# Kernel tuning notes

Hardware: AMD Instinct MI355X
Metric: run time of the kernel (lower is better)

Reference implementation:

```python
import jax, jax.numpy as jnp
import numpy as np

NUM_HEADS = 16
HEAD_DIM = 64
SCALE = HEAD_DIM ** -0.5


def setup_inputs() -> dict:
    key = jax.random.key(0)
    ks = jax.random.split(key, 5)
    B, N, C = 2, 2048, 1024
    x = jax.random.normal(ks[0], (B, N, C), dtype=jnp.float32)
    rel_pos_bias = jax.random.normal(ks[1], (NUM_HEADS, N, N), dtype=jnp.float32) * 0.02
    qkv_w = jax.random.normal(ks[2], (3 * C, C), dtype=jnp.float32) * (C ** -0.5)
    q_bias = jnp.zeros((C,), dtype=jnp.float32)
    v_bias = jnp.zeros((C,), dtype=jnp.float32)
    proj_w = jax.random.normal(ks[3], (C, C), dtype=jnp.float32) * (C ** -0.5)
    proj_b = jnp.zeros((C,), dtype=jnp.float32)
    return {"x": x, "rel_pos_bias": rel_pos_bias, "qkv_w": qkv_w,
            "q_bias": q_bias, "v_bias": v_bias, "proj_w": proj_w, "proj_b": proj_b}


def reference(x, rel_pos_bias, qkv_w, q_bias, v_bias, proj_w, proj_b):
    B, N, C = x.shape
    H, D = NUM_HEADS, HEAD_DIM
    # qkv bias = concat(q_bias, zeros, v_bias)
    qkv_b = jnp.concatenate([q_bias, jnp.zeros_like(v_bias), v_bias])
    qkv = x @ qkv_w.T + qkv_b                       # [B, N, 3C]
    qkv = qkv.reshape(B, N, 3, H, D).transpose(2, 0, 3, 1, 4)  # [3, B, H, N, D]
    q, k, v = qkv[0], qkv[1], qkv[2]
    q = q * SCALE
    attn = jnp.einsum('bhnd,bhmd->bhnm', q, k)      # [B, H, N, N]
    attn = attn + rel_pos_bias[None]                # bias broadcast over batch
    attn = jax.nn.softmax(attn, axis=-1)
    out = jnp.einsum('bhnm,bhmd->bhnd', attn, v)    # [B, H, N, D]
    out = out.transpose(0, 2, 1, 3).reshape(B, N, H * D)
    out = out @ proj_w.T + proj_b
    return out
```

## Files before the change

### kernel.cpp

```cpp
#include <hip/hip_runtime.h>

typedef unsigned short u16;
typedef short bfrag __attribute__((ext_vector_type(8)));
typedef float facc  __attribute__((ext_vector_type(4)));

#define LOG2E 1.44269504088896340736f

static __device__ __forceinline__ float bf2f(u16 b) {
  union { unsigned u; float f; } v; v.u = ((unsigned)b) << 16; return v.f;
}
static __device__ __forceinline__ u16 f2bf(float x) {
  union { float f; unsigned u; } v; v.f = x;
  return (u16)((v.u + 0x7FFFu + ((v.u >> 16) & 1u)) >> 16);
}
static __device__ __forceinline__ void gload_lds16(const u16* g, u16* l) {
  __builtin_amdgcn_global_load_lds((const __attribute__((address_space(1))) void*)g,
                                   (__attribute__((address_space(3))) void*)l,
                                   16, 0, 0);
}
static __device__ __forceinline__ void gload_lds16f(const float* g, float* l) {
  __builtin_amdgcn_global_load_lds((const __attribute__((address_space(1))) void*)g,
                                   (__attribute__((address_space(3))) void*)l,
                                   16, 0, 0);
}

__global__ __launch_bounds__(256) void convert_kernel(
    const float* __restrict__ x, const float* __restrict__ qw, const float* __restrict__ pw,
    u16* __restrict__ xb, u16* __restrict__ qwb, u16* __restrict__ pwb)
{
  const int NX = 4 * 1024 * 1024, NQ = 3 * 1024 * 1024, NP = 1024 * 1024;
  const int total4 = (NX + NQ + NP) >> 2;
  for (int i = blockIdx.x * blockDim.x + threadIdx.x; i < total4;
       i += gridDim.x * blockDim.x) {
    const int e = i << 2;
    const float* s; u16* d; int off;
    if (e < NX)            { s = x;  d = xb;  off = e; }
    else if (e < NX + NQ)  { s = qw; d = qwb; off = e - NX; }
    else                   { s = pw; d = pwb; off = e - NX - NQ; }
    float4 v = *(const float4*)(s + off);
    ushort4 o;
    o.x = f2bf(v.x); o.y = f2bf(v.y); o.z = f2bf(v.z); o.w = f2bf(v.w);
    *(ushort4*)(d + off) = o;
  }
}

static __device__ __forceinline__ void gemm128_bt(
    const u16* __restrict__ A, const u16* __restrict__ B, int K,
    int m0, int n0, u16* As, u16* Bs, facc acc[4][4])
{
  const int lane = threadIdx.x & 63;
  const int wv   = threadIdx.x >> 6;
  const int quad = lane >> 4;
  const int l15  = lane & 15;
  const int wm = wv >> 1, wn = wv & 1;
  const int srow = lane >> 2;
  const int skb  = (lane & 3) * 8;

  facc zero = {0.f, 0.f, 0.f, 0.f};
#pragma unroll
  for (int i = 0; i < 4; ++i)
#pragma unroll
    for (int j = 0; j < 4; ++j) acc[i][j] = zero;

  const int nIter = K >> 5;
  for (int kk = 0; kk < nIter; ++kk) {
    const int k0 = kk << 5;
    __syncthreads();
#pragma unroll
    for (int c = 0; c < 2; ++c) {
      const int seg = wv * 2 + c;
      gload_lds16(A + (long)(m0 + seg * 16 + srow) * K + k0 + skb, As + seg * 512);
      gload_lds16(B + (long)(n0 + seg * 16 + srow) * K + k0 + skb, Bs + seg * 512);
    }
    __syncthreads();
    bfrag af[4], bf[4];
#pragma unroll
    for (int i = 0; i < 4; ++i)
      af[i] = *(const bfrag*)(As + (wm * 64 + i * 16 + l15) * 32 + quad * 8);
#pragma unroll
    for (int j = 0; j < 4; ++j)
      bf[j] = *(const bfrag*)(Bs + (wn * 64 + j * 16 + l15) * 32 + quad * 8);
#pragma unroll
    for (int i = 0; i < 4; ++i)
#pragma unroll
      for (int j = 0; j < 4; ++j)
        acc[i][j] = __builtin_amdgcn_mfma_f32_16x16x32_bf16(af[i], bf[j], acc[i][j], 0, 0, 0);
  }
}

__global__ __launch_bounds__(256) void qkv_gemm_kernel(
    const u16* __restrict__ x, const u16* __restrict__ w,
    const float* __restrict__ qb, const float* __restrict__ vb,
    u16* __restrict__ Q, u16* __restrict__ Kd, u16* __restrict__ Vt)
{
  __shared__ u16 As[128 * 32];
  __shared__ u16 Bs[128 * 32];
  facc acc[4][4];
  const int m0 = blockIdx.y * 128;
  const int n0 = blockIdx.x * 128;
  gemm128_bt(x, w, 1024, m0, n0, As, Bs, acc);

  const int lane = threadIdx.x & 63;
  const int wv = threadIdx.x >> 6;
  const int quad = lane >> 4, l15 = lane & 15;
  const int wm = wv >> 1, wn = wv & 1;
  const int ncb = n0 + wn * 64;
  const int which = ncb >> 10;
  const int h = (ncb >> 6) & 15;

#pragma unroll
  for (int j = 0; j < 4; ++j) {
    const int d = j * 16 + l15;
    const int n_g = ncb + d;
#pragma unroll
    for (int i = 0; i < 4; ++i) {
      const int mg0 = m0 + wm * 64 + i * 16 + quad * 4;
      const int b  = mg0 >> 11;
      const int ns = mg0 & 2047;
      if (which == 0) {
        const float qbv = qb[n_g];
#pragma unroll
        for (int r = 0; r < 4; ++r)
          Q[(((long)(b * 16 + h) * 2048 + ns + r) << 6) + d] =
              f2bf((acc[i][j][r] + qbv) * 0.125f);
      } else if (which == 1) {
#pragma unroll
        for (int r = 0; r < 4; ++r)
          Kd[(((long)(b * 16 + h) * 2048 + ns + r) << 6) + d] = f2bf(acc[i][j][r]);
      } else {
        const float vbv = vb[n_g - 2048];
        ushort4 pk;
        pk.x = f2bf(acc[i][j][0] + vbv);
        pk.y = f2bf(acc[i][j][1] + vbv);
        pk.z = f2bf(acc[i][j][2] + vbv);
        pk.w = f2bf(acc[i][j][3] + vbv);
        *(ushort4*)(Vt + (((long)((b * 16 + h) * 64 + d)) << 11) + ns) = pk;
      }
    }
  }
}

__global__ __launch_bounds__(256, 4) void attn_kernel(
    const u16* __restrict__ Q, const u16* __restrict__ Kd, const u16* __restrict__ Vt,
    const float* __restrict__ bias, u16* __restrict__ AO)
{
  __shared__ u16 P[4][16 * 64];
  __shared__ float BiasS[4][2][16 * 64];
  const int lane = threadIdx.x & 63;
  const int wv = threadIdx.x >> 6;
  const int quad = lane >> 4, l15 = lane & 15;
  int bid = blockIdx.x;
  bid = (bid & 7) * 128 + (bid >> 3);
  const int bh = bid >> 5;
  const int qt = bid & 31;
  const int h = bh & 15;
  const int b = bh >> 4;
  const int q0 = qt * 64 + wv * 16;
  const long baseN = (long)bh << 17;

  bfrag qf0 = *(const bfrag*)(Q + baseN + (long)(q0 + l15) * 64 + quad * 8);
  bfrag qf1 = *(const bfrag*)(Q + baseN + (long)(q0 + l15) * 64 + 32 + quad * 8);

  facc o[4];
  float m_i[4], l_i[4];
  facc zero = {0.f, 0.f, 0.f, 0.f};
#pragma unroll
  for (int t = 0; t < 4; ++t) o[t] = zero;
#pragma unroll
  for (int r = 0; r < 4; ++r) { m_i[r] = -1e30f; l_i[r] = 0.f; }

  const float* brow = bias + ((long)h << 22) + ((long)q0 << 11);
  char* PwB = (char*)&P[wv][0];
  float* bS[2] = { &BiasS[wv][0][0], &BiasS[wv][1][0] };

#pragma unroll
  for (int c = 0; c < 4; ++c)
    gload_lds16f(brow + (long)(c * 4 + quad) * 2048 + l15 * 4, bS[0] + c * 256);

  for (int k0 = 0; k0 < 2048; k0 += 64) {
    const float* bsCur = bS[(k0 >> 6) & 1];
    facc s[4];
#pragma unroll
    for (int kt = 0; kt < 4; ++kt) {
      const u16* kb = Kd + baseN + (long)(k0 + kt * 16 + l15) * 64;
      bfrag kf0 = *(const bfrag*)(kb + quad * 8);
      bfrag kf1 = *(const bfrag*)(kb + 32 + quad * 8);
      facc z = zero;
      z = __builtin_amdgcn_mfma_f32_16x16x32_bf16(qf0, kf0, z, 0, 0, 0);
      z = __builtin_amdgcn_mfma_f32_16x16x32_bf16(qf1, kf1, z, 0, 0, 0);
      s[kt] = z;
    }
    asm volatile("s_waitcnt vmcnt(0)" ::: "memory");
#pragma unroll
    for (int kt = 0; kt < 4; ++kt)
#pragma unroll
      for (int r = 0; r < 4; ++r)
        s[kt][r] += bsCur[(quad * 4 + r) * 64 + kt * 16 + l15];

    if (k0 + 64 < 2048) {
      float* bsNxt = bS[((k0 >> 6) + 1) & 1];
      const float* src = brow + k0 + 64;
#pragma unroll
      for (int c = 0; c < 4; ++c)
        gload_lds16f(src + (long)(c * 4 + quad) * 2048 + l15 * 4, bsNxt + c * 256);
    }

    float alpha[4];
#pragma unroll
    for (int r = 0; r < 4; ++r) {
      float v = fmaxf(fmaxf(s[0][r], s[1][r]), fmaxf(s[2][r], s[3][r]));
      v = fmaxf(v, __shfl_xor(v, 1, 16));
      v = fmaxf(v, __shfl_xor(v, 2, 16));
      v = fmaxf(v, __shfl_xor(v, 4, 16));
      v = fmaxf(v, __shfl_xor(v, 8, 16));
      const float mn = fmaxf(m_i[r], v);
      alpha[r] = exp2f((m_i[r] - mn) * LOG2E);
      m_i[r] = mn;
    }
#pragma unroll
    for (int r = 0; r < 4; ++r) {
      const float p0 = exp2f((s[0][r] - m_i[r]) * LOG2E);
      const float p1 = exp2f((s[1][r] - m_i[r]) * LOG2E);
      const float p2 = exp2f((s[2][r] - m_i[r]) * LOG2E);
      const float p3 = exp2f((s[3][r] - m_i[r]) * LOG2E);
      s[0][r] = p0; s[1][r] = p1; s[2][r] = p2; s[3][r] = p3;
      float v = (p0 + p1) + (p2 + p3);
      v += __shfl_xor(v, 1, 16);
      v += __shfl_xor(v, 2, 16);
      v += __shfl_xor(v, 4, 16);
      v += __shfl_xor(v, 8, 16);
      l_i[r] = l_i[r] * alpha[r] + v;
    }
#pragma unroll
    for (int t = 0; t < 4; ++t)
#pragma unroll
      for (int r = 0; r < 4; ++r) o[t][r] *= alpha[r];

#pragma unroll
    for (int kt = 0; kt < 4; ++kt)
#pragma unroll
      for (int r = 0; r < 4; ++r) {
        const int bo = (kt * 2 + (l15 >> 3)) * 256 + (quad * 4 + r) * 16 + (l15 & 7) * 2;
        *(u16*)(PwB + bo) = f2bf(s[kt][r]);
      }

#pragma unroll
    for (int p = 0; p < 2; ++p) {
      bfrag pfp = *(const bfrag*)(PwB + p * 1024 + lane * 16);
#pragma unroll
      for (int t = 0; t < 4; ++t) {
        bfrag vf = *(const bfrag*)(Vt + baseN + (((long)(t * 16 + l15)) << 11)
                                   + k0 + p * 32 + quad * 8);
        o[t] = __builtin_amdgcn_mfma_f32_16x16x32_bf16(pfp, vf, o[t], 0, 0, 0);
      }
    }
  }

#pragma unroll
  for (int r = 0; r < 4; ++r) l_i[r] = 1.0f / l_i[r];
#pragma unroll
  for (int t = 0; t < 4; ++t)
#pragma unroll
    for (int r = 0; r < 4; ++r) {
      const int row = q0 + quad * 4 + r;
      AO[(((long)(b * 2048 + row)) << 10) + h * 64 + t * 16 + l15] = f2bf(o[t][r] * l_i[r]);
    }
}

__global__ __launch_bounds__(256) void proj_kernel(
    const u16* __restrict__ Ain, const u16* __restrict__ w,
    const float* __restrict__ pb, float* __restrict__ out)
{
  __shared__ u16 As[128 * 32];
  __shared__ u16 Bs[128 * 32];
  facc acc[4][4];
  const int m0 = blockIdx.y * 128;
  const int n0 = blockIdx.x * 128;
  gemm128_bt(Ain, w, 1024, m0, n0, As, Bs, acc);

  const int lane = threadIdx.x & 63;
  const int wv = threadIdx.x >> 6;
  const int quad = lane >> 4, l15 = lane & 15;
  const int wm = wv >> 1, wn = wv & 1;
#pragma unroll
  for (int j = 0; j < 4; ++j) {
    const int n_g = n0 + wn * 64 + j * 16 + l15;
    const float pbv = pb[n_g];
#pragma unroll
    for (int i = 0; i < 4; ++i) {
      const int mg0 = m0 + wm * 64 + i * 16 + quad * 4;
#pragma unroll
      for (int r = 0; r < 4; ++r)
        out[(((long)(mg0 + r)) << 10) + n_g] = acc[i][j][r] + pbv;
    }
  }
}

extern "C" void kernel_launch(void* const* d_in, const int* in_sizes, int n_in,
                              void* d_out, int out_size, void* d_ws, size_t ws_size,
                              hipStream_t stream)
{
  const float* x    = (const float*)d_in[0];
  const float* bias = (const float*)d_in[1];
  const float* qkvw = (const float*)d_in[2];
  const float* qb   = (const float*)d_in[3];
  const float* vb   = (const float*)d_in[4];
  const float* pw   = (const float*)d_in[5];
  const float* pb   = (const float*)d_in[6];
  float* out = (float*)d_out;

  char* ws = (char*)d_ws;
  u16* Q    = (u16*)(ws);
  u16* Kd   = (u16*)(ws + (size_t)8  * 1024 * 1024);
  u16* Vt   = (u16*)(ws + (size_t)16 * 1024 * 1024);
  u16* AO   = (u16*)(ws + (size_t)24 * 1024 * 1024);
  u16* xb   = (u16*)(ws + (size_t)32 * 1024 * 1024);
  u16* qwb  = (u16*)(ws + (size_t)40 * 1024 * 1024);
  u16* pwb  = (u16*)(ws + (size_t)46 * 1024 * 1024);

  hipLaunchKernelGGL(convert_kernel, dim3(1024), dim3(256), 0, stream,
                     x, qkvw, pw, xb, qwb, pwb);
  hipLaunchKernelGGL(qkv_gemm_kernel, dim3(24, 32), dim3(256), 0, stream,
                     xb, qwb, qb, vb, Q, Kd, Vt);
  hipLaunchKernelGGL(attn_kernel, dim3(1024), dim3(256), 0, stream,
                     Q, Kd, Vt, bias, AO);
  hipLaunchKernelGGL(proj_kernel, dim3(8, 32), dim3(256), 0, stream,
                     AO, pwb, pb, out);
}
```

Measured before the change: 671.8 us.

## Split attention over key halves, share bias across batch, add combine kernel

The attention kernel now splits the key dimension in two (split-K) and writes unnormalized partial outputs plus max and sum to a workspace. A new combine kernel merges them into the bf16 attention output. Each block pairs the two batch elements for the same head and query rows so the rel_pos_bias tile is loaded once and shared, using a swizzled LDS layout, non-temporal loads and a block-wide barrier. Occupancy is raised to 8 waves per SIMD. This trades an extra kernel launch and a partial-output round trip for more parallelism and half the bias traffic.

```diff
diff --git a/kernel.cpp b/kernel.cpp
--- a/kernel.cpp
+++ b/kernel.cpp
@@ -6,9 +6,6 @@
 
 #define LOG2E 1.44269504088896340736f
 
-static __device__ __forceinline__ float bf2f(u16 b) {
-  union { unsigned u; float f; } v; v.u = ((unsigned)b) << 16; return v.f;
-}
 static __device__ __forceinline__ u16 f2bf(float x) {
   union { float f; unsigned u; } v; v.f = x;
   return (u16)((v.u + 0x7FFFu + ((v.u >> 16) & 1u)) >> 16);
@@ -18,10 +15,10 @@
                                    (__attribute__((address_space(3))) void*)l,
                                    16, 0, 0);
 }
-static __device__ __forceinline__ void gload_lds16f(const float* g, float* l) {
+static __device__ __forceinline__ void gload_lds16f_nt(const float* g, float* l) {
   __builtin_amdgcn_global_load_lds((const __attribute__((address_space(1))) void*)g,
                                    (__attribute__((address_space(3))) void*)l,
-                                   16, 0, 0);
+                                   16, 0, 2);
 }
 
 __global__ __launch_bounds__(256) void convert_kernel(
@@ -140,26 +137,29 @@
   }
 }
 
-__global__ __launch_bounds__(256, 4) void attn_kernel(
+__global__ __launch_bounds__(256, 8) void attn_kernel(
     const u16* __restrict__ Q, const u16* __restrict__ Kd, const u16* __restrict__ Vt,
-    const float* __restrict__ bias, u16* __restrict__ AO)
+    const float* __restrict__ bias, float* __restrict__ Part)
 {
   __shared__ u16 P[4][16 * 64];
-  __shared__ float BiasS[4][2][16 * 64];
+  __shared__ float BiasS[2][2][16 * 64];
   const int lane = threadIdx.x & 63;
   const int wv = threadIdx.x >> 6;
   const int quad = lane >> 4, l15 = lane & 15;
-  int bid = blockIdx.x;
-  bid = (bid & 7) * 128 + (bid >> 3);
-  const int bh = bid >> 5;
-  const int qt = bid & 31;
-  const int h = bh & 15;
-  const int b = bh >> 4;
-  const int q0 = qt * 64 + wv * 16;
+  const int L  = (blockIdx.x & 7) * 256 + (blockIdx.x >> 3);
+  const int h  = L >> 7;
+  const int ks = (L >> 6) & 1;
+  const int qg = L & 63;
+  const int q0 = qg * 32;
+  const int b  = wv & 1;
+  const int qh = wv >> 1;
+  const int bh = b * 16 + h;
+  const int qw = q0 + qh * 16;
+  const int ksBase = ks << 10;
   const long baseN = (long)bh << 17;
 
-  bfrag qf0 = *(const bfrag*)(Q + baseN + (long)(q0 + l15) * 64 + quad * 8);
-  bfrag qf1 = *(const bfrag*)(Q + baseN + (long)(q0 + l15) * 64 + 32 + quad * 8);
+  bfrag qf0 = *(const bfrag*)(Q + baseN + (long)(qw + l15) * 64 + quad * 8);
+  bfrag qf1 = *(const bfrag*)(Q + baseN + (long)(qw + l15) * 64 + 32 + quad * 8);
 
   facc o[4];
   float m_i[4], l_i[4];
@@ -169,16 +169,26 @@
 #pragma unroll
   for (int r = 0; r < 4; ++r) { m_i[r] = -1e30f; l_i[r] = 0.f; }
 
-  const float* brow = bias + ((long)h << 22) + ((long)q0 << 11);
+  const float* bh_bias = bias + ((long)h << 22) + ((long)q0 << 11);
   char* PwB = (char*)&P[wv][0];
-  float* bS[2] = { &BiasS[wv][0][0], &BiasS[wv][1][0] };
-
-#pragma unroll
-  for (int c = 0; c < 4; ++c)
-    gload_lds16f(brow + (long)(c * 4 + quad) * 2048 + l15 * 4, bS[0] + c * 256);
-
-  for (int k0 = 0; k0 < 2048; k0 += 64) {
-    const float* bsCur = bS[(k0 >> 6) & 1];
+
+  auto stage = [&](int buf, int kk) {
+#pragma unroll
+    for (int cc = 0; cc < 2; ++cc) {
+      const int c_ = b * 2 + cc;
+      const int row_ = c_ * 4 + quad;
+      gload_lds16f_nt(bh_bias + (long)(qh * 16 + row_) * 2048 + kk
+                        + ((l15 * 4) ^ ((row_ & 7) << 2)),
+                      &BiasS[buf][qh][0] + c_ * 256);
+    }
+  };
+
+  stage(0, ksBase);
+
+  for (int it = 0; it < 16; ++it) {
+    const int k0 = ksBase + it * 64;
+    __syncthreads();
+
     facc s[4];
 #pragma unroll
     for (int kt = 0; kt < 4; ++kt) {
@@ -190,20 +200,17 @@
       z = __builtin_amdgcn_mfma_f32_16x16x32_bf16(qf1, kf1, z, 0, 0, 0);
       s[kt] = z;
     }
-    asm volatile("s_waitcnt vmcnt(0)" ::: "memory");
+
+    const float* bs = &BiasS[it & 1][qh][0];
 #pragma unroll
     for (int kt = 0; kt < 4; ++kt)
 #pragma unroll
-      for (int r = 0; r < 4; ++r)
-        s[kt][r] += bsCur[(quad * 4 + r) * 64 + kt * 16 + l15];
-
-    if (k0 + 64 < 2048) {
-      float* bsNxt = bS[((k0 >> 6) + 1) & 1];
-      const float* src = brow + k0 + 64;
-#pragma unroll
-      for (int c = 0; c < 4; ++c)
-        gload_lds16f(src + (long)(c * 4 + quad) * 2048 + l15 * 4, bsNxt + c * 256);
-    }
+      for (int r = 0; r < 4; ++r) {
+        const int row = quad * 4 + r;
+        s[kt][r] += bs[row * 64 + ((kt * 16 + l15) ^ ((row & 7) << 2))];
+      }
+
+    if (it + 1 < 16) stage((it + 1) & 1, k0 + 64);
 
     float alpha[4];
 #pragma unroll
@@ -256,15 +263,37 @@
     }
   }
 
-#pragma unroll
-  for (int r = 0; r < 4; ++r) l_i[r] = 1.0f / l_i[r];
+  const long prBase = ((long)ks * 65536 + (long)bh * 2048 + qw) * 80;
 #pragma unroll
   for (int t = 0; t < 4; ++t)
 #pragma unroll
-    for (int r = 0; r < 4; ++r) {
-      const int row = q0 + quad * 4 + r;
-      AO[(((long)(b * 2048 + row)) << 10) + h * 64 + t * 16 + l15] = f2bf(o[t][r] * l_i[r]);
-    }
+    for (int r = 0; r < 4; ++r)
+      Part[prBase + (long)(quad * 4 + r) * 80 + t * 16 + l15] = o[t][r];
+#pragma unroll
+  for (int r = 0; r < 4; ++r)
+    if (l15 < 2)
+      Part[prBase + (long)(quad * 4 + r) * 80 + 64 + l15] = (l15 == 0) ? m_i[r] : l_i[r];
+}
+
+__global__ __launch_bounds__(256) void combine_kernel(
+    const float* __restrict__ Part, u16* __restrict__ AO)
+{
+  const int lane = threadIdx.x & 63;
+  const int wv = threadIdx.x >> 6;
+  const long row = (long)blockIdx.x * 4 + wv;
+  const int bh = (int)(row >> 11);
+  const int q  = (int)(row & 2047);
+  const int b = bh >> 4, h = bh & 15;
+  const float* p0 = Part + row * 80;
+  const float* p1 = Part + (row + 65536) * 80;
+  const float o0 = p0[lane], o1 = p1[lane];
+  const float m0 = p0[64], l0 = p0[65];
+  const float m1 = p1[64], l1 = p1[65];
+  const float m = fmaxf(m0, m1);
+  const float w0 = exp2f((m0 - m) * LOG2E);
+  const float w1 = exp2f((m1 - m) * LOG2E);
+  const float ov = (o0 * w0 + o1 * w1) / (l0 * w0 + l1 * w1);
+  AO[(((long)(b * 2048 + q)) << 10) + h * 64 + lane] = f2bf(ov);
 }
 
 __global__ __launch_bounds__(256) void proj_kernel(
@@ -317,13 +346,16 @@
   u16* xb   = (u16*)(ws + (size_t)32 * 1024 * 1024);
   u16* qwb  = (u16*)(ws + (size_t)40 * 1024 * 1024);
   u16* pwb  = (u16*)(ws + (size_t)46 * 1024 * 1024);
+  float* Part = (float*)(ws + (size_t)48 * 1024 * 1024);
 
   hipLaunchKernelGGL(convert_kernel, dim3(1024), dim3(256), 0, stream,
                      x, qkvw, pw, xb, qwb, pwb);
   hipLaunchKernelGGL(qkv_gemm_kernel, dim3(24, 32), dim3(256), 0, stream,
                      xb, qwb, qb, vb, Q, Kd, Vt);
-  hipLaunchKernelGGL(attn_kernel, dim3(1024), dim3(256), 0, stream,
-                     Q, Kd, Vt, bias, AO);
+  hipLaunchKernelGGL(attn_kernel, dim3(2048), dim3(256), 0, stream,
+                     Q, Kd, Vt, bias, Part);
+  hipLaunchKernelGGL(combine_kernel, dim3(16384), dim3(256), 0, stream,
+                     Part, AO);
   hipLaunchKernelGGL(proj_kernel, dim3(8, 32), dim3(256), 0, stream,
                      AO, pwb, pb, out);
 }
```

Measured after the change: 656.8 us. -2.2%, faster.
